# Performance work log

Measured on AMD Instinct MI355X. Metric: run time of the kernel, lower is better.

The kernel has to match this reference:

```python
import jax, jax.numpy as jnp
import numpy as np


def _layernorm(x, g, b, eps=1e-5):
    m = x.mean(-1, keepdims=True)
    v = ((x - m) ** 2).mean(-1, keepdims=True)
    return (x - m) * jax.lax.rsqrt(v + eps) * g + b


def _silu(x):
    return x * jax.nn.sigmoid(x)


def _mamba_mixer(x, in_w, conv_w, conv_b, xp_w, dt_w, dt_b, A_log, Dp, out_w):
    # x: (B, L, C) ; HF Mamba slow-path math
    B, L, C = x.shape
    dI = in_w.shape[0] // 2
    h, gate = jnp.split(x @ in_w.T, 2, axis=-1)  # (B, L, dI) each
    hc = jnp.transpose(h, (0, 2, 1))             # (B, dI, L)
    K = conv_w.shape[-1]
    hc = jax.lax.conv_general_dilated(hc, conv_w, (1,), [(K - 1, 0)],
                                      feature_group_count=dI,
                                      dimension_numbers=('NCH', 'OIH', 'NCH'))
    hc = _silu(hc + conv_b[None, :, None])
    u = jnp.transpose(hc, (0, 2, 1))             # (B, L, dI)
    R = dt_w.shape[1]
    N = A_log.shape[1]
    dt, Bs, Cs = jnp.split(u @ xp_w.T, [R, R + N], axis=-1)
    dt = jax.nn.softplus(dt @ dt_w.T + dt_b)     # (B, L, dI)
    A = -jnp.exp(A_log)                          # (dI, N)
    dA = jnp.exp(dt[..., None] * A)              # (B, L, dI, N)
    dBu = dt[..., None] * Bs[:, :, None, :] * u[..., None]  # (B, L, dI, N)

    def step(state, inp):
        dA_t, dBu_t, C_t = inp
        state = dA_t * state + dBu_t             # (B, dI, N)
        y = jnp.einsum('bdn,bn->bd', state, C_t)
        return state, y

    h0 = jnp.zeros((B, dI, N), x.dtype)
    _, ys = jax.lax.scan(step, h0, (jnp.swapaxes(dA, 0, 1),
                                    jnp.swapaxes(dBu, 0, 1),
                                    jnp.swapaxes(Cs, 0, 1)))
    y = jnp.swapaxes(ys, 0, 1)                   # (B, L, dI)
    y = (y + u * Dp) * _silu(gate)
    return y @ out_w.T


def _mixffn(x, H, W, fc1_w, fc1_b, pe_w, pe_b, fc2_w, fc2_b):
    B, L, C = x.shape
    img = jnp.transpose(x, (0, 2, 1)).reshape(B, C, H, W)
    t = jnp.einsum('bchw,fc->bfhw', img, fc1_w[:, :, 0, 0]) + fc1_b[None, :, None, None]
    Fch = pe_w.shape[0]
    t = jax.lax.conv_general_dilated(t, pe_w, (1, 1), [(1, 1), (1, 1)],
                                     feature_group_count=Fch,
                                     dimension_numbers=('NCHW', 'OIHW', 'NCHW'))
    t = t + pe_b[None, :, None, None]
    t = jax.nn.gelu(t, approximate=False)
    t = jnp.einsum('bfhw,cf->bchw', t, fc2_w[:, :, 0, 0]) + fc2_b[None, :, None, None]
    return jnp.transpose(t.reshape(B, C, L), (0, 2, 1))


def _forward(x, norm1_g, norm1_b, in_w, conv_w, conv_b, xp_w, dt_w, dt_b, A_log, Dp,
             out_w, norm2_g, norm2_b, gate_w, fc1_w, fc1_b, pe_w, pe_b, fc2_w, fc2_b,
             rand_index, H, W):
    identity = x
    B = x.shape[0]
    x_in = jnp.concatenate([x, jnp.flip(x, 1), x[:, rand_index]], axis=0)  # (3B, L, C)
    xn = _layernorm(x_in, norm1_g, norm1_b)
    y = _mamba_mixer(xn, in_w, conv_w, conv_b, xp_w, dt_w, dt_b, A_log, Dp, out_w)
    fwd, rev, shf = jnp.split(y, 3, axis=0)
    rev = jnp.flip(rev, 1)
    inv = jnp.argsort(rand_index)
    shf = shf[:, inv]
    g_in = jnp.concatenate([fwd.mean(1), rev.mean(1), shf.mean(1)], axis=-1)  # (B, 3C)
    g = jax.nn.softmax(g_in @ gate_w.T, axis=-1)                              # (B, 3)
    y = g[:, 0, None, None] * fwd + g[:, 1, None, None] * rev + g[:, 2, None, None] * shf
    x1 = identity + y
    xn2 = _layernorm(x1, norm2_g, norm2_b)
    return x1 + _mixffn(xn2, H, W, fc1_w, fc1_b, pe_w, pe_b, fc2_w, fc2_b)


def setup_inputs() -> dict:
    B, H, W, C = 2, 64, 64, 128
    L = H * W
    dI, N, K, R, Fch = 384, 4, 4, 128, 512
    key = jax.random.key(0)
    ks = jax.random.split(key, 32)
    s = lambda i, shape, sc=0.02: jax.random.normal(ks[i], shape, jnp.float32) * sc
    A_log = jnp.log(jnp.broadcast_to(jnp.arange(1, N + 1, dtype=jnp.float32), (dI, N)))
    return {
        'x': jax.random.normal(ks[0], (B, L, C), jnp.float32),
        'rand_index': jax.random.permutation(ks[1], L),
        'H': H, 'W': W,
        'norm1_g': jnp.ones((C,), jnp.float32),
        'norm1_b': jnp.zeros((C,), jnp.float32),
        'in_w': s(2, (2 * dI, C)),
        'conv_w': s(3, (dI, 1, K), 0.1),
        'conv_b': jnp.zeros((dI,), jnp.float32),
        'xp_w': s(4, (R + 2 * N, dI)),
        'dt_w': s(5, (dI, R)),
        'dt_b': s(6, (dI,), 0.1),
        'A_log': A_log,
        'Dp': jnp.ones((dI,), jnp.float32),
        'out_w': s(7, (C, dI)),
        'norm2_g': jnp.ones((C,), jnp.float32),
        'norm2_b': jnp.zeros((C,), jnp.float32),
        'gate_w': s(8, (3, 3 * C)),
        'fc1_w': s(9, (Fch, C, 1, 1)),
        'fc1_b': jnp.zeros((Fch,), jnp.float32),
        'pe_w': s(10, (Fch, 1, 3, 3), 0.1),
        'pe_b': jnp.zeros((Fch,), jnp.float32),
        'fc2_w': s(11, (C, Fch, 1, 1)),
        'fc2_b': jnp.zeros((C,), jnp.float32),
    }


def reference(x, rand_index, H, W, norm1_g, norm1_b, in_w, conv_w, conv_b, xp_w,
              dt_w, dt_b, A_log, Dp, out_w, norm2_g, norm2_b, gate_w,
              fc1_w, fc1_b, pe_w, pe_b, fc2_w, fc2_b):
    return _forward(x, norm1_g, norm1_b, in_w, conv_w, conv_b, xp_w, dt_w, dt_b,
                    A_log, Dp, out_w, norm2_g, norm2_b, gate_w, fc1_w, fc1_b,
                    pe_w, pe_b, fc2_w, fc2_b, rand_index, H, W)
```

## Files before the change

kernel.cpp:

```cpp
#include <hip/hip_runtime.h>
#include <math.h>

#define LLEN 4096
#define CCH 128
#define DI 384
#define NST 4
#define SBN 6
#define NB 2
#define FCH 512
#define NCHUNK 128
#define TSTEP 32

typedef short bf16x8 __attribute__((ext_vector_type(8)));
typedef short bf16x4 __attribute__((ext_vector_type(4)));
typedef float f32x4 __attribute__((ext_vector_type(4)));
typedef float f32x8 __attribute__((ext_vector_type(8)));

__device__ __forceinline__ float wave_sum(float v) {
#pragma unroll
    for (int o = 32; o > 0; o >>= 1) v += __shfl_xor(v, o);
    return v;
}

__device__ __forceinline__ short f2bf(float f) {
    unsigned int u = __float_as_uint(f);
    unsigned int r = (u + 0x7fffu + ((u >> 16) & 1u)) >> 16;
    return (short)r;
}
__device__ __forceinline__ float bf2f(short s) {
    return __uint_as_float(((unsigned int)(unsigned short)s) << 16);
}

#define OFF_IN  0
#define OFF_DTC 98304
#define OFF_BC  245760
#define OFF_OUT 248832
#define OFF_FC1 297984
#define OFF_FC2 363520
#define OFF_END 429056
#define NCONV   281600
#define NCBLK   1100

__global__ __launch_bounds__(256) void conv_comp(const float* __restrict__ in_w,
                                                 const float* __restrict__ xp_w,
                                                 const float* __restrict__ dt_w,
                                                 const float* __restrict__ out_w,
                                                 const float* __restrict__ fc1_w,
                                                 const float* __restrict__ fc2_w,
                                                 short* __restrict__ wb)
{
    int bid = blockIdx.x;
    if (bid < NCBLK) {
        int i = bid * 256 + threadIdx.x;
        if (i >= NCONV) return;
        int idx = (i < OFF_DTC) ? i : i + (OFF_OUT - OFF_DTC);
        float v;
        if (idx < OFF_DTC)      v = in_w[idx];
        else if (idx < OFF_OUT) v = xp_w[128 * 384 + (idx - OFF_BC)];
        else if (idx < OFF_FC1) v = out_w[idx - OFF_OUT];
        else if (idx < OFF_FC2) v = fc1_w[idx - OFF_FC1];
        else                    v = fc2_w[idx - OFF_FC2];
        wb[idx] = f2bf(v);
    } else {
        int ji = (bid - NCBLK) * 256 + threadIdx.x;
        int j = ji / 384, k = ji % 384;
        float acc = 0.f;
#pragma unroll 8
        for (int n = 0; n < 128; n++)
            acc += dt_w[j * 128 + n] * xp_w[n * 384 + k];
        wb[OFF_DTC + j * 384 + k] = f2bf(acc);
    }
}

__global__ __launch_bounds__(256) void prep_ln1(const float* __restrict__ x,
                                                const float* __restrict__ g,
                                                const float* __restrict__ b,
                                                short* __restrict__ xn)
{
    int r = blockIdx.x * 4 + (threadIdx.x >> 6);
    int lane = threadIdx.x & 63;
    const float* src = x + (size_t)r * CCH;
    float v0 = src[lane], v1 = src[lane + 64];
    float m = wave_sum(v0 + v1) * (1.f / 128.f);
    float d0 = v0 - m, d1 = v1 - m;
    float var = wave_sum(d0 * d0 + d1 * d1) * (1.f / 128.f);
    float rstd = rsqrtf(var + 1e-5f);
    short* dst = xn + (size_t)r * CCH;
    dst[lane]      = f2bf(d0 * rstd * g[lane]      + b[lane]);
    dst[lane + 64] = f2bf(d1 * rstd * g[lane + 64] + b[lane + 64]);
}

template<int EPI>
__global__ __launch_bounds__(256) void gemm_w(const short* __restrict__ A, int lda,
                                              const short* __restrict__ W, int ldw, int Ntot,
                                              const float* __restrict__ bias,
                                              const float* __restrict__ res, int ldr,
                                              float* __restrict__ C0,
                                              short* __restrict__ Cb, int ldc,
                                              float* __restrict__ extra,
                                              int Kd)
{
    __shared__ short Als[64 * 72];
    __shared__ short Wls[128 * 72];
    int tid = threadIdx.x;
    int wid = tid >> 6, lane = tid & 63;
    int wm = wid >> 1, wn = wid & 1;
    int l15 = lane & 15, l4 = lane >> 4;
    int bm = blockIdx.x * 64, bn = blockIdx.y * 128;
    int srow = tid >> 3, scol = (tid & 7) * 8;
    f32x4 acc[2][4] = {};
    for (int k0 = 0; k0 < Kd; k0 += 64) {
        bf16x8 av0 = *(const bf16x8*)&A[(size_t)(bm + srow) * lda + k0 + scol];
        bf16x8 av1 = *(const bf16x8*)&A[(size_t)(bm + srow + 32) * lda + k0 + scol];
        bf16x8 wv[4];
#pragma unroll
        for (int q = 0; q < 4; q++) {
            if (EPI == 7) {
                wv[q] = bf16x8{};
                if (bn + srow + 32 * q < Ntot)
                    wv[q] = *(const bf16x8*)&W[(size_t)(bn + srow + 32 * q) * ldw + k0 + scol];
            } else {
                wv[q] = *(const bf16x8*)&W[(size_t)(bn + srow + 32 * q) * ldw + k0 + scol];
            }
        }
        __syncthreads();
        *(bf16x8*)&Als[srow * 72 + scol] = av0;
        *(bf16x8*)&Als[(srow + 32) * 72 + scol] = av1;
#pragma unroll
        for (int q = 0; q < 4; q++)
            *(bf16x8*)&Wls[(srow + 32 * q) * 72 + scol] = wv[q];
        __syncthreads();
#pragma unroll
        for (int ks = 0; ks < 2; ks++) {
            bf16x8 af[2], bw[4];
#pragma unroll
            for (int f = 0; f < 2; f++)
                af[f] = *(const bf16x8*)&Als[(wm * 32 + f * 16 + l15) * 72 + ks * 32 + l4 * 8];
#pragma unroll
            for (int j = 0; j < 4; j++)
                bw[j] = *(const bf16x8*)&Wls[(wn * 64 + j * 16 + l15) * 72 + ks * 32 + l4 * 8];
#pragma unroll
            for (int i = 0; i < 2; i++)
#pragma unroll
                for (int j = 0; j < 4; j++)
                    acc[i][j] = __builtin_amdgcn_mfma_f32_16x16x32_bf16(af[i], bw[j], acc[i][j], 0, 0, 0);
        }
    }
    __shared__ float cs[128];
    if (EPI == 8) {
        if (tid < 128) cs[tid] = 0.f;
        __syncthreads();
    }
#pragma unroll
    for (int i = 0; i < 2; i++) {
        int row0 = bm + wm * 32 + i * 16 + l4 * 4;
#pragma unroll
        for (int j = 0; j < 4; j++) {
            int col = bn + wn * 64 + j * 16 + l15;
            if (EPI == 7) {
                if (col < 384) {
                    float bv = bias[col];
#pragma unroll
                    for (int r = 0; r < 4; r++) {
                        float v = acc[i][j][r] + bv;
                        v = (v > 20.f) ? v : __logf(1.f + __expf(v));
                        Cb[(size_t)(row0 + r) * ldc + col] = f2bf(v);
                    }
                } else if (col < 392) {
#pragma unroll
                    for (int r = 0; r < 4; r++)
                        extra[(size_t)(row0 + r) * 8 + (col - 384)] = acc[i][j][r];
                }
            } else {
                float bv = (EPI == 3 || EPI == 6) ? bias[col] : 0.f;
                float csum = 0.f;
#pragma unroll
                for (int r = 0; r < 4; r++) {
                    float v = acc[i][j][r] + bv;
                    if (EPI == 3) v += res[(size_t)(row0 + r) * ldr + col];
                    if (EPI == 5 || EPI == 6)
                        Cb[(size_t)(row0 + r) * ldc + col] = f2bf(v);
                    else
                        C0[(size_t)(row0 + r) * ldc + col] = v;
                    csum += v;
                }
                if (EPI == 8) atomicAdd(&cs[wn * 64 + j * 16 + l15], csum);
            }
        }
    }
    if (EPI == 8) {
        __syncthreads();
        if (tid < 128) atomicAdd(&extra[(bm >> 12) * 128 + tid], cs[tid]);
    }
}

__global__ __launch_bounds__(192) void dwconv_silu_v3(const short* __restrict__ hg,
                                                      const int* __restrict__ ridx,
                                                      const float* __restrict__ cw,
                                                      const float* __restrict__ cb,
                                                      short* __restrict__ ub)
{
    int t = threadIdx.x;
    int c = t % 48, rs = t / 48;
    int blk = blockIdx.x;
    int sb = blk >> 7;
    int s = sb >> 1, bb = sb & 1;
    int l0 = ((blk & 127) << 5) + rs * 8;
    int d0 = c * 8;
    float w0[8], w1[8], w2[8], w3[8], bs[8];
#pragma unroll
    for (int e = 0; e < 8; e++) {
        int d = d0 + e;
        bs[e] = cb[d];
        w0[e] = cw[d * 4 + 0]; w1[e] = cw[d * 4 + 1];
        w2[e] = cw[d * 4 + 2]; w3[e] = cw[d * 4 + 3];
    }
    float r0[8], r1[8], r2[8];
#pragma unroll
    for (int e = 0; e < 8; e++) { r0[e] = 0.f; r1[e] = 0.f; r2[e] = 0.f; }
    if (l0 - 3 >= 0) {
        int j = l0 - 3;
        int sl = (s == 0) ? j : (s == 1 ? LLEN - 1 - j : ridx[j]);
        bf16x8 v = *(const bf16x8*)&hg[(size_t)(bb * LLEN + sl) * 768 + d0];
#pragma unroll
        for (int e = 0; e < 8; e++) r0[e] = bf2f(v[e]);
    }
    if (l0 - 2 >= 0) {
        int j = l0 - 2;
        int sl = (s == 0) ? j : (s == 1 ? LLEN - 1 - j : ridx[j]);
        bf16x8 v = *(const bf16x8*)&hg[(size_t)(bb * LLEN + sl) * 768 + d0];
#pragma unroll
        for (int e = 0; e < 8; e++) r1[e] = bf2f(v[e]);
    }
    if (l0 - 1 >= 0) {
        int j = l0 - 1;
        int sl = (s == 0) ? j : (s == 1 ? LLEN - 1 - j : ridx[j]);
        bf16x8 v = *(const bf16x8*)&hg[(size_t)(bb * LLEN + sl) * 768 + d0];
#pragma unroll
        for (int e = 0; e < 8; e++) r2[e] = bf2f(v[e]);
    }
#pragma unroll
    for (int i = 0; i < 8; i++) {
        int j = l0 + i;
        int sl = (s == 0) ? j : (s == 1 ? LLEN - 1 - j : ridx[j]);
        bf16x8 v = *(const bf16x8*)&hg[(size_t)(bb * LLEN + sl) * 768 + d0];
        float r3[8];
#pragma unroll
        for (int e = 0; e < 8; e++) r3[e] = bf2f(v[e]);
        bf16x8 ov;
#pragma unroll
        for (int e = 0; e < 8; e++) {
            float a = bs[e] + w0[e] * r0[e] + w1[e] * r1[e] + w2[e] * r2[e] + w3[e] * r3[e];
            ov[e] = f2bf(a * __builtin_amdgcn_rcpf(1.f + __expf(-a)));
        }
        *(bf16x8*)&ub[(size_t)(sb * LLEN + j) * DI + d0] = ov;
#pragma unroll
        for (int e = 0; e < 8; e++) { r0[e] = r1[e]; r1[e] = r2[e]; r2[e] = r3[e]; }
    }
}

__global__ __launch_bounds__(DI) void scan_phaseA2(const short* __restrict__ dtb,
                                                   const float* __restrict__ bc,
                                                   const short* __restrict__ ub,
                                                   const float* __restrict__ A_log,
                                                   float* __restrict__ PS)
{
    __shared__ short ds_dt[TSTEP * DI];
    __shared__ short ds_u[TSTEP * DI];
    __shared__ float ds_bc[TSTEP * 8];
    int tid = threadIdx.x;
    int bid = blockIdx.x;
    int sb = bid / NCHUNK, chunk = bid % NCHUNK;
    int base = sb * LLEN + chunk * TSTEP;
    {
        int rr = tid / 48, cc = (tid % 48) * 8;
#pragma unroll
        for (int p = 0; p < 4; p++) {
            int row = p * 8 + rr;
            *(bf16x8*)&ds_dt[row * DI + cc] = *(const bf16x8*)&dtb[(size_t)(base + row) * DI + cc];
            *(bf16x8*)&ds_u[row * DI + cc]  = *(const bf16x8*)&ub[(size_t)(base + row) * DI + cc];
        }
        if (tid < TSTEP * 8) ds_bc[tid] = bc[(size_t)base * 8 + tid];
    }
    int d = tid;
    f32x4 al = *(const f32x4*)&A_log[d * 4];
    float a[NST];
#pragma unroll
    for (int n = 0; n < NST; n++) a[n] = -__expf(al[n]);
    __syncthreads();
    float s[NST] = {0.f, 0.f, 0.f, 0.f}, p[NST] = {1.f, 1.f, 1.f, 1.f};
    for (int t = 0; t < TSTEP; t++) {
        float dtv = bf2f(ds_dt[t * DI + d]);
        float dtu = dtv * bf2f(ds_u[t * DI + d]);
#pragma unroll
        for (int n = 0; n < NST; n++) {
            float dA = __expf(dtv * a[n]);
            s[n] = dA * s[n] + dtu * ds_bc[t * 8 + n];
            p[n] *= dA;
        }
    }
    f32x8 v;
#pragma unroll
    for (int n = 0; n < NST; n++) { v[2 * n] = p[n]; v[2 * n + 1] = s[n]; }
    *(f32x8*)&PS[(size_t)(sb * NCHUNK + chunk) * 3072 + d * 8] = v;
}

__global__ __launch_bounds__(256) void scan_phaseB2(const float* __restrict__ PS,
                                                    float* __restrict__ I)
{
    int gid = blockIdx.x * 256 + threadIdx.x;
    if (gid >= SBN * 1536) return;
    int sb = gid / 1536, dn = gid % 1536;
    const float* ps = PS + (size_t)sb * NCHUNK * 3072 + dn * 2;
    float* Ip = I + (size_t)sb * NCHUNK * 1536 + dn;
    float st = 0.f;
    for (int c = 0; c < NCHUNK; c += 8) {
        float2 v[8];
#pragma unroll
        for (int q = 0; q < 8; q++) v[q] = *(const float2*)&ps[(size_t)(c + q) * 3072];
#pragma unroll
        for (int q = 0; q < 8; q++) { Ip[(size_t)(c + q) * 1536] = st; st = v[q].x * st + v[q].y; }
    }
}

__global__ __launch_bounds__(DI) void scan_phaseC2(const short* __restrict__ dtb,
                                                   const float* __restrict__ bc,
                                                   const short* __restrict__ ub,
                                                   const short* __restrict__ hg,
                                                   const int* __restrict__ ridx,
                                                   const float* __restrict__ A_log,
                                                   const float* __restrict__ Dp,
                                                   const float* __restrict__ I,
                                                   short* __restrict__ ymix)
{
    __shared__ short ds_dt[TSTEP * DI];
    __shared__ short ds_u[TSTEP * DI];
    __shared__ float ds_bc[TSTEP * 8];
    __shared__ int ds_src[TSTEP];
    int tid = threadIdx.x;
    int bid = blockIdx.x;
    int sb = bid / NCHUNK, chunk = bid % NCHUNK;
    int s2 = sb >> 1, bb = sb & 1;
    int base = sb * LLEN + chunk * TSTEP;
    {
        int rr = tid / 48, cc = (tid % 48) * 8;
#pragma unroll
        for (int p = 0; p < 4; p++) {
            int row = p * 8 + rr;
            *(bf16x8*)&ds_dt[row * DI + cc] = *(const bf16x8*)&dtb[(size_t)(base + row) * DI + cc];
            *(bf16x8*)&ds_u[row * DI + cc]  = *(const bf16x8*)&ub[(size_t)(base + row) * DI + cc];
        }
        if (tid < TSTEP * 8) ds_bc[tid] = bc[(size_t)base * 8 + tid];
        if (tid < TSTEP) {
            int l = chunk * TSTEP + tid;
            int sl = (s2 == 0) ? l : (s2 == 1 ? LLEN - 1 - l : ridx[l]);
            ds_src[tid] = bb * LLEN + sl;
        }
    }
    int d = tid;
    f32x4 al = *(const f32x4*)&A_log[d * 4];
    float a[NST];
#pragma unroll
    for (int n = 0; n < NST; n++) a[n] = -__expf(al[n]);
    __syncthreads();
    float s[NST];
    {
        f32x4 si = *(const f32x4*)&I[(size_t)(sb * NCHUNK + chunk) * 1536 + d * 4];
#pragma unroll
        for (int n = 0; n < NST; n++) s[n] = si[n];
    }
    float Dv = Dp[d];
    for (int t = 0; t < TSTEP; t++) {
        float dtv = bf2f(ds_dt[t * DI + d]);
        float uv = bf2f(ds_u[t * DI + d]);
        float dtu = dtv * uv;
        float y = 0.f;
#pragma unroll
        for (int n = 0; n < NST; n++) {
            float dA = __expf(dtv * a[n]);
            s[n] = dA * s[n] + dtu * ds_bc[t * 8 + n];
            y += s[n] * ds_bc[t * 8 + 4 + n];
        }
        float gt = bf2f(hg[(size_t)ds_src[t] * 768 + 384 + d]);
        float sg = gt * __builtin_amdgcn_rcpf(1.f + __expf(-gt));
        ymix[(size_t)(base + t) * DI + d] = f2bf((y + uv * Dv) * sg);
    }
}

__global__ __launch_bounds__(384) void gate_inv(const float* __restrict__ means,
                                                const float* __restrict__ gw,
                                                float* __restrict__ g,
                                                const int* __restrict__ ridx,
                                                int* __restrict__ inv)
{
    if (blockIdx.x == 0) {
        int lane = threadIdx.x & 63, p = threadIdx.x >> 6;
        int bb = p / 3, j = p % 3;
        float part = 0.f;
        for (int i = lane; i < 384; i += 64) {
            int s = i >> 7, c = i & 127;
            part += means[(s * 2 + bb) * 128 + c] * (1.f / 4096.f) * gw[j * 384 + i];
        }
        part = wave_sum(part);
        __shared__ float lg[6];
        if (lane == 0) lg[p] = part;
        __syncthreads();
        if (threadIdx.x < 2) {
            int b2 = threadIdx.x;
            float a0 = lg[b2 * 3], a1 = lg[b2 * 3 + 1], a2 = lg[b2 * 3 + 2];
            float mx = fmaxf(a0, fmaxf(a1, a2));
            float e0 = __expf(a0 - mx), e1 = __expf(a1 - mx), e2 = __expf(a2 - mx);
            float iv = __builtin_amdgcn_rcpf(e0 + e1 + e2);
            g[b2 * 3] = e0 * iv; g[b2 * 3 + 1] = e1 * iv; g[b2 * 3 + 2] = e2 * iv;
        }
    } else {
        if (threadIdx.x < 256) {
            int l = (blockIdx.x - 1) * 256 + threadIdx.x;
            inv[ridx[l]] = l;
        }
    }
}

__global__ __launch_bounds__(256) void combine_ln2(const float* __restrict__ x,
                                                   const float* __restrict__ y6,
                                                   const float* __restrict__ g,
                                                   const int* __restrict__ inv,
                                                   const float* __restrict__ n2g,
                                                   const float* __restrict__ n2b,
                                                   float* __restrict__ x1,
                                                   short* __restrict__ xn2)
{
    int r = blockIdx.x * 4 + (threadIdx.x >> 6);
    int lane = threadIdx.x & 63;
    int bb = r / LLEN, l = r % LLEN;
    float g0 = g[bb * 3 + 0], g1 = g[bb * 3 + 1], g2 = g[bb * 3 + 2];
    int il = inv[l];
    size_t fo = ((size_t)(0 + bb) * LLEN + l) * CCH;
    size_t ro = ((size_t)(2 + bb) * LLEN + (LLEN - 1 - l)) * CCH;
    size_t so = ((size_t)(4 + bb) * LLEN + il) * CCH;
    size_t xo = ((size_t)bb * LLEN + l) * CCH;
    float v0 = x[xo + lane]      + g0 * y6[fo + lane]      + g1 * y6[ro + lane]      + g2 * y6[so + lane];
    float v1 = x[xo + lane + 64] + g0 * y6[fo + lane + 64] + g1 * y6[ro + lane + 64] + g2 * y6[so + lane + 64];
    float m = wave_sum(v0 + v1) * (1.f / 128.f);
    float d0 = v0 - m, d1 = v1 - m;
    float var = wave_sum(d0 * d0 + d1 * d1) * (1.f / 128.f);
    float rstd = rsqrtf(var + 1e-5f);
    x1[xo + lane] = v0; x1[xo + lane + 64] = v1;
    xn2[xo + lane]      = f2bf(d0 * rstd * n2g[lane]      + n2b[lane]);
    xn2[xo + lane + 64] = f2bf(d1 * rstd * n2g[lane + 64] + n2b[lane + 64]);
}

__global__ __launch_bounds__(256) void peconv_gelu_v2(const short* __restrict__ t,
                                                      const float* __restrict__ pw,
                                                      const float* __restrict__ pb,
                                                      short* __restrict__ t2)
{
    int tid = threadIdx.x;
    int fc = tid & 127;
    int wsr = tid >> 7;
    int blk = blockIdx.x;
    int whalf = blk & 1, h = (blk >> 1) & 63, bb = blk >> 7;
    int w0 = whalf * 32 + wsr * 16;
    int f0 = fc * 4;
    float wt[9][4], bias4[4];
#pragma unroll
    for (int e = 0; e < 4; e++) {
        bias4[e] = pb[f0 + e];
#pragma unroll
        for (int k = 0; k < 9; k++) wt[k][e] = pw[(f0 + e) * 9 + k];
    }
    size_t base = (size_t)bb * 4096 * FCH;
    float cm1[3][4], cc[3][4], cn[3][4];
#pragma unroll
    for (int rr = 0; rr < 3; rr++)
#pragma unroll
        for (int e = 0; e < 4; e++) { cm1[rr][e] = 0.f; cc[rr][e] = 0.f; }
#pragma unroll
    for (int rr = 0; rr < 3; rr++) {
        int hh = h + rr - 1;
        if (hh >= 0 && hh < 64) {
            if (w0 - 1 >= 0) {
                bf16x4 v = *(const bf16x4*)&t[base + ((size_t)hh * 64 + (w0 - 1)) * FCH + f0];
#pragma unroll
                for (int e = 0; e < 4; e++) cm1[rr][e] = bf2f(v[e]);
            }
            bf16x4 v = *(const bf16x4*)&t[base + ((size_t)hh * 64 + w0) * FCH + f0];
#pragma unroll
            for (int e = 0; e < 4; e++) cc[rr][e] = bf2f(v[e]);
        }
    }
#pragma unroll
    for (int i = 0; i < 16; i++) {
        int w = w0 + i;
#pragma unroll
        for (int rr = 0; rr < 3; rr++) {
#pragma unroll
            for (int e = 0; e < 4; e++) cn[rr][e] = 0.f;
            int hh = h + rr - 1;
            if (hh >= 0 && hh < 64 && w + 1 < 64) {
                bf16x4 v = *(const bf16x4*)&t[base + ((size_t)hh * 64 + (w + 1)) * FCH + f0];
#pragma unroll
                for (int e = 0; e < 4; e++) cn[rr][e] = bf2f(v[e]);
            }
        }
        bf16x4 ov;
#pragma unroll
        for (int e = 0; e < 4; e++) {
            float acc = bias4[e];
#pragma unroll
            for (int rr = 0; rr < 3; rr++) {
                acc += wt[rr * 3 + 0][e] * cm1[rr][e];
                acc += wt[rr * 3 + 1][e] * cc[rr][e];
                acc += wt[rr * 3 + 2][e] * cn[rr][e];
            }
            ov[e] = f2bf(0.5f * acc * (1.f + erff(acc * 0.70710678118654752f)));
        }
        *(bf16x4*)&t2[base + ((size_t)h * 64 + w) * FCH + f0] = ov;
#pragma unroll
        for (int rr = 0; rr < 3; rr++)
#pragma unroll
            for (int e = 0; e < 4; e++) { cm1[rr][e] = cc[rr][e]; cc[rr][e] = cn[rr][e]; }
    }
}

extern "C" void kernel_launch(void* const* d_in, const int* in_sizes, int n_in,
                              void* d_out, int out_size, void* d_ws, size_t ws_size,
                              hipStream_t stream)
{
    (void)in_sizes; (void)n_in; (void)ws_size; (void)out_size;
    const float* x      = (const float*)d_in[0];
    const int*   ridx   = (const int*)d_in[1];
    const float* n1g    = (const float*)d_in[4];
    const float* n1b    = (const float*)d_in[5];
    const float* in_w   = (const float*)d_in[6];
    const float* conv_w = (const float*)d_in[7];
    const float* conv_b = (const float*)d_in[8];
    const float* xp_w   = (const float*)d_in[9];
    const float* dt_w   = (const float*)d_in[10];
    const float* dt_b   = (const float*)d_in[11];
    const float* A_log  = (const float*)d_in[12];
    const float* Dp     = (const float*)d_in[13];
    const float* out_w  = (const float*)d_in[14];
    const float* n2g    = (const float*)d_in[15];
    const float* n2b    = (const float*)d_in[16];
    const float* gate_w = (const float*)d_in[17];
    const float* fc1_w  = (const float*)d_in[18];
    const float* fc1_b  = (const float*)d_in[19];
    const float* pe_w   = (const float*)d_in[20];
    const float* pe_b   = (const float*)d_in[21];
    const float* fc2_w  = (const float*)d_in[22];
    const float* fc2_b  = (const float*)d_in[23];
    float* out = (float*)d_out;

    float* ws = (float*)d_ws;
    short* wb   = (short*)ws;
    float* regA = ws + 215040;
    float* regB = regA + 2097152;
    float* regC = regB + 9437184;
    float* regD = regC + 4718592;
    float* regE = regD + 4718592;
    float* regF = regE + 4718592;
    float* regG = regF + 2359296;
    float* smallb = regG + 196608;

    short* xn   = (short*)regA;
    float* Ibuf = regA;
    short* tbuf = (short*)regA;
    short* hg   = (short*)regB;
    float* y6   = regB;
    float* x1   = regB + 3145728;
    short* xn2  = (short*)(regB + 4194304);
    short* t2   = (short*)(regB + 4718592);
    short* ub   = (short*)regC;
    short* ymix = (short*)regD;
    short* dtb  = (short*)regE;
    float* PS   = regF;
    float* xpbc = regG;
    float* means = smallb;
    float* gbuf  = smallb + 768;
    int*   invb  = (int*)(gbuf + 8);

    const int M6 = SBN * LLEN;
    const int M2 = NB * LLEN;

    conv_comp<<<NCBLK + 576, 256, 0, stream>>>(in_w, xp_w, dt_w, out_w, fc1_w, fc2_w, wb);
    hipMemsetAsync(means, 0, 768 * sizeof(float), stream);
    prep_ln1<<<M2 / 4, 256, 0, stream>>>(x, n1g, n1b, xn);
    gemm_w<5><<<dim3(M2 / 64, 6), 256, 0, stream>>>(xn, CCH, wb + OFF_IN, CCH, 768, nullptr, nullptr, 0, nullptr, hg, 768, nullptr, CCH);
    dwconv_silu_v3<<<768, 192, 0, stream>>>(hg, ridx, conv_w, conv_b, ub);
    gemm_w<7><<<dim3(M6 / 64, 4), 256, 0, stream>>>(ub, DI, wb + OFF_DTC, DI, 392, dt_b, nullptr, 0, nullptr, dtb, DI, xpbc, DI);
    scan_phaseA2<<<SBN * NCHUNK, DI, 0, stream>>>(dtb, xpbc, ub, A_log, PS);
    scan_phaseB2<<<36, 256, 0, stream>>>(PS, Ibuf);
    scan_phaseC2<<<SBN * NCHUNK, DI, 0, stream>>>(dtb, xpbc, ub, hg, ridx, A_log, Dp, Ibuf, ymix);
    gemm_w<8><<<dim3(M6 / 64, 1), 256, 0, stream>>>(ymix, DI, wb + OFF_OUT, DI, CCH, nullptr, nullptr, 0, y6, nullptr, CCH, means, DI);
    gate_inv<<<17, 384, 0, stream>>>(means, gate_w, gbuf, ridx, invb);
    combine_ln2<<<M2 / 4, 256, 0, stream>>>(x, y6, gbuf, invb, n2g, n2b, x1, xn2);
    gemm_w<6><<<dim3(M2 / 64, 4), 256, 0, stream>>>(xn2, CCH, wb + OFF_FC1, CCH, FCH, fc1_b, nullptr, 0, nullptr, tbuf, FCH, nullptr, CCH);
    peconv_gelu_v2<<<256, 256, 0, stream>>>(tbuf, pe_w, pe_b, t2);
    gemm_w<3><<<dim3(M2 / 64, 1), 256, 0, stream>>>(t2, FCH, wb + OFF_FC2, FCH, CCH, fc2_b, x1, CCH, out, nullptr, CCH, nullptr, FCH);
}
```

Before: 183.0 us.

## Fold gated three-way combine before out-projection and compute gate means from pre-projection sums

Uses the linearity of the out-projection to apply the softmax gate weights to the three scan outputs before projecting, so one GEMM over the combined rows replaces a GEMM over all six sequences plus a float y6 buffer. The gate means are now computed by accumulating per-channel column sums inside the scan kernel, then projecting them through out_w in the gate kernel. The combine, out-projection, residual add and LayerNorm2 are fused into one MFMA kernel. This removes a memset, one kernel launch and the large y6 write and read, at the cost of a gather of three ymix rows per output row, bf16 rounding of the combined activations, and global atomics in the scan.

```diff
diff --git a/kernel.cpp b/kernel.cpp
--- a/kernel.cpp
+++ b/kernel.cpp
@@ -47,7 +47,8 @@
                                                  const float* __restrict__ out_w,
                                                  const float* __restrict__ fc1_w,
                                                  const float* __restrict__ fc2_w,
-                                                 short* __restrict__ wb)
+                                                 short* __restrict__ wb,
+                                                 float* __restrict__ colsum)
 {
     int bid = blockIdx.x;
     if (bid < NCBLK) {
@@ -62,6 +63,9 @@
         else                    v = fc2_w[idx - OFF_FC2];
         wb[idx] = f2bf(v);
     } else {
+        if (bid == NCBLK) {
+            for (int i = threadIdx.x; i < SBN * DI; i += 256) colsum[i] = 0.f;
+        }
         int ji = (bid - NCBLK) * 256 + threadIdx.x;
         int j = ji / 384, k = ji % 384;
         float acc = 0.f;
@@ -146,11 +150,6 @@
                     acc[i][j] = __builtin_amdgcn_mfma_f32_16x16x32_bf16(af[i], bw[j], acc[i][j], 0, 0, 0);
         }
     }
-    __shared__ float cs[128];
-    if (EPI == 8) {
-        if (tid < 128) cs[tid] = 0.f;
-        __syncthreads();
-    }
 #pragma unroll
     for (int i = 0; i < 2; i++) {
         int row0 = bm + wm * 32 + i * 16 + l4 * 4;
@@ -173,7 +172,6 @@
                 }
             } else {
                 float bv = (EPI == 3 || EPI == 6) ? bias[col] : 0.f;
-                float csum = 0.f;
 #pragma unroll
                 for (int r = 0; r < 4; r++) {
                     float v = acc[i][j][r] + bv;
@@ -182,15 +180,9 @@
                         Cb[(size_t)(row0 + r) * ldc + col] = f2bf(v);
                     else
                         C0[(size_t)(row0 + r) * ldc + col] = v;
-                    csum += v;
                 }
-                if (EPI == 8) atomicAdd(&cs[wn * 64 + j * 16 + l15], csum);
             }
         }
-    }
-    if (EPI == 8) {
-        __syncthreads();
-        if (tid < 128) atomicAdd(&extra[(bm >> 12) * 128 + tid], cs[tid]);
     }
 }
 
@@ -323,7 +315,7 @@
     }
 }
 
-__global__ __launch_bounds__(DI) void scan_phaseC2(const short* __restrict__ dtb,
+__global__ __launch_bounds__(DI) void scan_phaseC3(const short* __restrict__ dtb,
                                                    const float* __restrict__ bc,
                                                    const short* __restrict__ ub,
                                                    const short* __restrict__ hg,
@@ -331,7 +323,8 @@
                                                    const float* __restrict__ A_log,
                                                    const float* __restrict__ Dp,
                                                    const float* __restrict__ I,
-                                                   short* __restrict__ ymix)
+                                                   short* __restrict__ ymix,
+                                                   float* __restrict__ colsum)
 {
     __shared__ short ds_dt[TSTEP * DI];
     __shared__ short ds_u[TSTEP * DI];
@@ -370,6 +363,7 @@
         for (int n = 0; n < NST; n++) s[n] = si[n];
     }
     float Dv = Dp[d];
+    float csum = 0.f;
     for (int t = 0; t < TSTEP; t++) {
         float dtv = bf2f(ds_dt[t * DI + d]);
         float uv = bf2f(ds_u[t * DI + d]);
@@ -383,30 +377,46 @@
         }
         float gt = bf2f(hg[(size_t)ds_src[t] * 768 + 384 + d]);
         float sg = gt * __builtin_amdgcn_rcpf(1.f + __expf(-gt));
-        ymix[(size_t)(base + t) * DI + d] = f2bf((y + uv * Dv) * sg);
-    }
-}
-
-__global__ __launch_bounds__(384) void gate_inv(const float* __restrict__ means,
-                                                const float* __restrict__ gw,
-                                                float* __restrict__ g,
-                                                const int* __restrict__ ridx,
-                                                int* __restrict__ inv)
+        float val = (y + uv * Dv) * sg;
+        ymix[(size_t)(base + t) * DI + d] = f2bf(val);
+        csum += val;
+    }
+    atomicAdd(&colsum[sb * DI + d], csum);
+}
+
+__global__ __launch_bounds__(384) void gate2(const float* __restrict__ colsum,
+                                             const float* __restrict__ out_w,
+                                             const float* __restrict__ gw,
+                                             float* __restrict__ g,
+                                             const int* __restrict__ ridx,
+                                             int* __restrict__ inv)
 {
     if (blockIdx.x == 0) {
-        int lane = threadIdx.x & 63, p = threadIdx.x >> 6;
-        int bb = p / 3, j = p % 3;
+        __shared__ float m6[768];
+        int tid = threadIdx.x;
+        for (int ii = tid; ii < 768; ii += 384) {
+            int sb = ii >> 7, c = ii & 127;
+            const float* cs = colsum + sb * 384;
+            const float* w = out_w + c * 384;
+            float acc = 0.f;
+#pragma unroll 4
+            for (int d = 0; d < 384; d++) acc += cs[d] * w[d];
+            m6[ii] = acc * (1.f / 4096.f);
+        }
+        __syncthreads();
+        int lane = tid & 63, p = tid >> 6;
+        int bb = p / 3, j2 = p % 3;
         float part = 0.f;
         for (int i = lane; i < 384; i += 64) {
-            int s = i >> 7, c = i & 127;
-            part += means[(s * 2 + bb) * 128 + c] * (1.f / 4096.f) * gw[j * 384 + i];
+            int j = i >> 7, c = i & 127;
+            part += m6[(j * 2 + bb) * 128 + c] * gw[j2 * 384 + i];
         }
         part = wave_sum(part);
         __shared__ float lg[6];
         if (lane == 0) lg[p] = part;
         __syncthreads();
-        if (threadIdx.x < 2) {
-            int b2 = threadIdx.x;
+        if (tid < 2) {
+            int b2 = tid;
             float a0 = lg[b2 * 3], a1 = lg[b2 * 3 + 1], a2 = lg[b2 * 3 + 2];
             float mx = fmaxf(a0, fmaxf(a1, a2));
             float e0 = __expf(a0 - mx), e1 = __expf(a1 - mx), e2 = __expf(a2 - mx);
@@ -421,33 +431,114 @@
     }
 }
 
-__global__ __launch_bounds__(256) void combine_ln2(const float* __restrict__ x,
-                                                   const float* __restrict__ y6,
-                                                   const float* __restrict__ g,
-                                                   const int* __restrict__ inv,
-                                                   const float* __restrict__ n2g,
-                                                   const float* __restrict__ n2b,
-                                                   float* __restrict__ x1,
-                                                   short* __restrict__ xn2)
-{
-    int r = blockIdx.x * 4 + (threadIdx.x >> 6);
-    int lane = threadIdx.x & 63;
-    int bb = r / LLEN, l = r % LLEN;
+__global__ __launch_bounds__(256) void combine_outproj_ln2(const short* __restrict__ ymix,
+                                                           const float* __restrict__ x,
+                                                           const float* __restrict__ g,
+                                                           const int* __restrict__ inv,
+                                                           const short* __restrict__ Wout,
+                                                           const float* __restrict__ n2g,
+                                                           const float* __restrict__ n2b,
+                                                           float* __restrict__ x1,
+                                                           short* __restrict__ xn2)
+{
+    __shared__ short Als[64 * 72];
+    __shared__ short Wls[128 * 72];
+    __shared__ float xs[64][132];
+    __shared__ int ssrc[192];
+    __shared__ float msh[64], rsh[64];
+    int tid = threadIdx.x;
+    int bm = blockIdx.x * 64;
+    int bb = bm >> 12;
+    if (tid < 64) {
+        int l = (bm & 4095) + tid;
+        ssrc[tid * 3 + 0] = bb * LLEN + l;
+        ssrc[tid * 3 + 1] = (2 + bb) * LLEN + (LLEN - 1 - l);
+        ssrc[tid * 3 + 2] = (4 + bb) * LLEN + inv[l];
+    }
     float g0 = g[bb * 3 + 0], g1 = g[bb * 3 + 1], g2 = g[bb * 3 + 2];
-    int il = inv[l];
-    size_t fo = ((size_t)(0 + bb) * LLEN + l) * CCH;
-    size_t ro = ((size_t)(2 + bb) * LLEN + (LLEN - 1 - l)) * CCH;
-    size_t so = ((size_t)(4 + bb) * LLEN + il) * CCH;
-    size_t xo = ((size_t)bb * LLEN + l) * CCH;
-    float v0 = x[xo + lane]      + g0 * y6[fo + lane]      + g1 * y6[ro + lane]      + g2 * y6[so + lane];
-    float v1 = x[xo + lane + 64] + g0 * y6[fo + lane + 64] + g1 * y6[ro + lane + 64] + g2 * y6[so + lane + 64];
-    float m = wave_sum(v0 + v1) * (1.f / 128.f);
-    float d0 = v0 - m, d1 = v1 - m;
-    float var = wave_sum(d0 * d0 + d1 * d1) * (1.f / 128.f);
-    float rstd = rsqrtf(var + 1e-5f);
-    x1[xo + lane] = v0; x1[xo + lane + 64] = v1;
-    xn2[xo + lane]      = f2bf(d0 * rstd * n2g[lane]      + n2b[lane]);
-    xn2[xo + lane + 64] = f2bf(d1 * rstd * n2g[lane + 64] + n2b[lane + 64]);
+    int wid = tid >> 6, lane = tid & 63;
+    int wm = wid >> 1, wn = wid & 1;
+    int l15 = lane & 15, l4 = lane >> 4;
+    int srow = tid >> 3, scol = (tid & 7) * 8;
+    __syncthreads();
+    f32x4 acc[2][4] = {};
+    for (int k0 = 0; k0 < DI; k0 += 64) {
+        bf16x8 cmb[2];
+#pragma unroll
+        for (int hh = 0; hh < 2; hh++) {
+            int r = srow + 32 * hh;
+            bf16x8 vf = *(const bf16x8*)&ymix[(size_t)ssrc[r * 3 + 0] * DI + k0 + scol];
+            bf16x8 vr = *(const bf16x8*)&ymix[(size_t)ssrc[r * 3 + 1] * DI + k0 + scol];
+            bf16x8 vs = *(const bf16x8*)&ymix[(size_t)ssrc[r * 3 + 2] * DI + k0 + scol];
+#pragma unroll
+            for (int e = 0; e < 8; e++)
+                cmb[hh][e] = f2bf(g0 * bf2f(vf[e]) + g1 * bf2f(vr[e]) + g2 * bf2f(vs[e]));
+        }
+        bf16x8 wv[4];
+#pragma unroll
+        for (int q = 0; q < 4; q++)
+            wv[q] = *(const bf16x8*)&Wout[(size_t)(srow + 32 * q) * DI + k0 + scol];
+        __syncthreads();
+        *(bf16x8*)&Als[srow * 72 + scol] = cmb[0];
+        *(bf16x8*)&Als[(srow + 32) * 72 + scol] = cmb[1];
+#pragma unroll
+        for (int q = 0; q < 4; q++)
+            *(bf16x8*)&Wls[(srow + 32 * q) * 72 + scol] = wv[q];
+        __syncthreads();
+#pragma unroll
+        for (int ks = 0; ks < 2; ks++) {
+            bf16x8 af[2], bw[4];
+#pragma unroll
+            for (int f = 0; f < 2; f++)
+                af[f] = *(const bf16x8*)&Als[(wm * 32 + f * 16 + l15) * 72 + ks * 32 + l4 * 8];
+#pragma unroll
+            for (int j = 0; j < 4; j++)
+                bw[j] = *(const bf16x8*)&Wls[(wn * 64 + j * 16 + l15) * 72 + ks * 32 + l4 * 8];
+#pragma unroll
+            for (int i = 0; i < 2; i++)
+#pragma unroll
+                for (int j = 0; j < 4; j++)
+                    acc[i][j] = __builtin_amdgcn_mfma_f32_16x16x32_bf16(af[i], bw[j], acc[i][j], 0, 0, 0);
+        }
+    }
+#pragma unroll
+    for (int i = 0; i < 2; i++) {
+        int rowl = wm * 32 + i * 16 + l4 * 4;
+#pragma unroll
+        for (int j = 0; j < 4; j++) {
+            int col = wn * 64 + j * 16 + l15;
+#pragma unroll
+            for (int r = 0; r < 4; r++)
+                xs[rowl + r][col] = acc[i][j][r] + x[(size_t)(bm + rowl + r) * CCH + col];
+        }
+    }
+    __syncthreads();
+    {
+        int row = tid >> 2, q = tid & 3;
+        float sum = 0.f, sq = 0.f;
+#pragma unroll
+        for (int c = q * 32; c < q * 32 + 32; c++) { float v = xs[row][c]; sum += v; sq += v * v; }
+        sum += __shfl_xor(sum, 1); sq += __shfl_xor(sq, 1);
+        sum += __shfl_xor(sum, 2); sq += __shfl_xor(sq, 2);
+        if (q == 0) {
+            float m = sum * (1.f / 128.f);
+            float var = sq * (1.f / 128.f) - m * m;
+            msh[row] = m;
+            rsh[row] = rsqrtf(fmaxf(var, 0.f) + 1e-5f);
+        }
+    }
+    __syncthreads();
+    {
+        int col = tid & 127;
+        float gg = n2g[col], b2 = n2b[col];
+#pragma unroll
+        for (int e = 0; e < 32; e++) {
+            int row = e * 2 + (tid >> 7);
+            float v = xs[row][col];
+            x1[(size_t)(bm + row) * CCH + col] = v;
+            xn2[(size_t)(bm + row) * CCH + col] = f2bf((v - msh[row]) * rsh[row] * gg + b2);
+        }
+    }
 }
 
 __global__ __launch_bounds__(256) void peconv_gelu_v2(const short* __restrict__ t,
@@ -567,7 +658,6 @@
     float* Ibuf = regA;
     short* tbuf = (short*)regA;
     short* hg   = (short*)regB;
-    float* y6   = regB;
     float* x1   = regB + 3145728;
     short* xn2  = (short*)(regB + 4194304);
     short* t2   = (short*)(regB + 4718592);
@@ -576,25 +666,23 @@
     short* dtb  = (short*)regE;
     float* PS   = regF;
     float* xpbc = regG;
-    float* means = smallb;
-    float* gbuf  = smallb + 768;
-    int*   invb  = (int*)(gbuf + 8);
+    float* colsum = smallb;
+    float* gbuf   = smallb + 2304;
+    int*   invb   = (int*)(gbuf + 8);
 
     const int M6 = SBN * LLEN;
     const int M2 = NB * LLEN;
 
-    conv_comp<<<NCBLK + 576, 256, 0, stream>>>(in_w, xp_w, dt_w, out_w, fc1_w, fc2_w, wb);
-    hipMemsetAsync(means, 0, 768 * sizeof(float), stream);
+    conv_comp<<<NCBLK + 576, 256, 0, stream>>>(in_w, xp_w, dt_w, out_w, fc1_w, fc2_w, wb, colsum);
     prep_ln1<<<M2 / 4, 256, 0, stream>>>(x, n1g, n1b, xn);
     gemm_w<5><<<dim3(M2 / 64, 6), 256, 0, stream>>>(xn, CCH, wb + OFF_IN, CCH, 768, nullptr, nullptr, 0, nullptr, hg, 768, nullptr, CCH);
     dwconv_silu_v3<<<768, 192, 0, stream>>>(hg, ridx, conv_w, conv_b, ub);
     gemm_w<7><<<dim3(M6 / 64, 4), 256, 0, stream>>>(ub, DI, wb + OFF_DTC, DI, 392, dt_b, nullptr, 0, nullptr, dtb, DI, xpbc, DI);
     scan_phaseA2<<<SBN * NCHUNK, DI, 0, stream>>>(dtb, xpbc, ub, A_log, PS);
     scan_phaseB2<<<36, 256, 0, stream>>>(PS, Ibuf);
-    scan_phaseC2<<<SBN * NCHUNK, DI, 0, stream>>>(dtb, xpbc, ub, hg, ridx, A_log, Dp, Ibuf, ymix);
-    gemm_w<8><<<dim3(M6 / 64, 1), 256, 0, stream>>>(ymix, DI, wb + OFF_OUT, DI, CCH, nullptr, nullptr, 0, y6, nullptr, CCH, means, DI);
-    gate_inv<<<17, 384, 0, stream>>>(means, gate_w, gbuf, ridx, invb);
-    combine_ln2<<<M2 / 4, 256, 0, stream>>>(x, y6, gbuf, invb, n2g, n2b, x1, xn2);
+    scan_phaseC3<<<SBN * NCHUNK, DI, 0, stream>>>(dtb, xpbc, ub, hg, ridx, A_log, Dp, Ibuf, ymix, colsum);
+    gate2<<<17, 384, 0, stream>>>(colsum, out_w, gate_w, gbuf, ridx, invb);
+    combine_outproj_ln2<<<M2 / 64, 256, 0, stream>>>(ymix, x, gbuf, invb, wb + OFF_OUT, n2g, n2b, x1, xn2);
     gemm_w<6><<<dim3(M2 / 64, 4), 256, 0, stream>>>(xn2, CCH, wb + OFF_FC1, CCH, FCH, fc1_b, nullptr, 0, nullptr, tbuf, FCH, nullptr, CCH);
     peconv_gelu_v2<<<256, 256, 0, stream>>>(tbuf, pe_w, pe_b, t2);
     gemm_w<3><<<dim3(M2 / 64, 1), 256, 0, stream>>>(t2, FCH, wb + OFF_FC2, FCH, CCH, fc2_b, x1, CCH, out, nullptr, CCH, nullptr, FCH);
```

Measured after the change: 217.7 us. +18.9%, slower.
